# Kernel tuning notes

Hardware: AMD Instinct MI355X
Metric: run time of the kernel (lower is better)

The kernel has to match this reference:

```python
import jax, jax.numpy as jnp
import numpy as np

N = 50000       # nodes
E = 800000      # edges (avg degree 16)
IN_F = 128
OUT_F = 128
NEG_SLOPE = 0.2  # LeakyReLU alpha
EPS = 1e-10


def setup_inputs() -> dict:
    key = jax.random.key(0)
    k1, k2, k3, k4 = jax.random.split(key, 4)
    h = jax.random.normal(k1, (N, IN_F), dtype=jnp.float32)
    edge_index = jax.random.randint(k2, (2, E), 0, N, dtype=jnp.int32)
    # nn.Linear(in, out, bias=False): weight is [out, in], Wh = h @ W.T
    W = jax.random.normal(k3, (OUT_F, IN_F), dtype=jnp.float32) * (1.0 / np.sqrt(IN_F))
    # a: [2*out, 1], xavier_uniform with gain=1.414
    lim = 1.414 * np.sqrt(6.0 / (2 * OUT_F + 1))
    a = jax.random.uniform(k4, (2 * OUT_F, 1), dtype=jnp.float32, minval=-lim, maxval=lim)
    return {"h": h, "edge_index": edge_index, "W": W, "a": a}


def reference(h, edge_index, W, a):
    Wh = h @ W.T                              # [N, out]
    rows = edge_index[0]
    cols = edge_index[1]
    # cat([Wh_i, Wh_j],1) @ a  ==  (Wh @ a1)[rows] + (Wh @ a2)[cols]
    a1 = a[:OUT_F, 0]
    a2 = a[OUT_F:, 0]
    s1 = Wh @ a1                              # [N]
    s2 = Wh @ a2                              # [N]
    e = jax.nn.leaky_relu(s1[rows] + s2[cols], negative_slope=NEG_SLOPE)  # [E]
    e = e - jnp.max(e)
    exp_e = jnp.exp(e)
    sum_exp = jax.ops.segment_sum(exp_e, rows, num_segments=N)            # [N]
    alpha = exp_e / (sum_exp[rows] + EPS)                                 # [E]
    # sparse.mm(adj_att, Wh): h_prime[i] = sum_j alpha_ij * Wh[j]
    h_prime = jax.ops.segment_sum(alpha[:, None] * Wh[cols], rows, num_segments=N)
    return jax.nn.elu(h_prime)
```

## Files before the change

kernel.cpp:

```cpp
#include <hip/hip_runtime.h>

constexpr int FD = 128;
constexpr int NBMAX = 512;
constexpr int CH1 = 2048;
constexpr int CAPB = 3072;

typedef __attribute__((ext_vector_type(8))) short short8;
typedef __attribute__((ext_vector_type(4))) float floatx4;

__device__ __forceinline__ unsigned fenc(float f) {
    unsigned u = __float_as_uint(f);
    return (u & 0x80000000u) ? ~u : (u | 0x80000000u);
}
__device__ __forceinline__ float fdec(unsigned e) {
    return (e & 0x80000000u) ? __uint_as_float(e & 0x7fffffffu)
                             : __uint_as_float(~e);
}

__device__ __forceinline__ unsigned bpack(float x, float y) {
    unsigned ux = __float_as_uint(x); ux += 0x7FFFu + ((ux >> 16) & 1u);
    unsigned uy = __float_as_uint(y); uy += 0x7FFFu + ((uy >> 16) & 1u);
    return (ux >> 16) | (uy & 0xFFFF0000u);
}

__global__ __launch_bounds__(128) void initwt_kernel(const float* __restrict__ W,
                                                     unsigned* __restrict__ Wb,
                                                     int* __restrict__ bhist,
                                                     unsigned* __restrict__ maxslot) {
    int j = blockIdx.x, k = threadIdx.x;
    float w = W[(size_t)j * FD + k];
    float pw = __shfl_xor(w, 1, 64);
    if ((k & 1) == 0) Wb[(size_t)j * 64 + (k >> 1)] = bpack(w, pw);
    if (j == 0) {
        for (int i = k; i < NBMAX; i += 128) bhist[i] = 0;
        if (k < 2) maxslot[k] = 0x007FFFFFu;
    }
}

__global__ __launch_bounds__(256) void gemm_kernel(const float* __restrict__ h,
                                                   const unsigned* __restrict__ Wb,
                                                   const float* __restrict__ a,
                                                   unsigned* __restrict__ Whb,
                                                   float* __restrict__ s1,
                                                   float* __restrict__ s2, int n) {
    int w = threadIdx.x >> 6, lane = threadIdx.x & 63;
    int quad = lane >> 4, c = lane & 15;
    int rbase = blockIdx.x * 64 + w * 16;

    int arow = min(rbase + c, n - 1);
    const float4* hrow = (const float4*)(h + (size_t)arow * FD);
    union { uint4 u; short8 s; } af[4];
#pragma unroll
    for (int kk = 0; kk < 4; ++kk) {
        int k0 = kk * 32 + quad * 8;
        float4 f0 = hrow[k0 >> 2];
        float4 f1 = hrow[(k0 >> 2) + 1];
        af[kk].u.x = bpack(f0.x, f0.y);
        af[kk].u.y = bpack(f0.z, f0.w);
        af[kk].u.z = bpack(f1.x, f1.y);
        af[kk].u.w = bpack(f1.z, f1.w);
    }

    float p1a[4] = {0.f, 0.f, 0.f, 0.f};
    float p2a[4] = {0.f, 0.f, 0.f, 0.f};

#pragma unroll
    for (int t = 0; t < 8; ++t) {
        const uint4* brow = (const uint4*)(Wb + (size_t)(t * 16 + c) * 64 + quad * 4);
        floatx4 acc = {0.f, 0.f, 0.f, 0.f};
#pragma unroll
        for (int kk = 0; kk < 4; ++kk) {
            union { uint4 u; short8 s; } bf;
            bf.u = brow[kk * 4];
            acc = __builtin_amdgcn_mfma_f32_16x16x32_bf16(af[kk].s, bf.s, acc, 0, 0, 0);
        }
        float a1v = a[t * 16 + c];
        float a2v = a[FD + t * 16 + c];
#pragma unroll
        for (int i = 0; i < 4; ++i) {
            float v = acc[i];
            p1a[i] = fmaf(v, a1v, p1a[i]);
            p2a[i] = fmaf(v, a2v, p2a[i]);
            float pv = __shfl_xor(v, 1, 64);
            int r = rbase + quad * 4 + i;
            if ((c & 1) == 0 && r < n)
                Whb[(size_t)r * 64 + t * 8 + (c >> 1)] = bpack(v, pv);
        }
    }

#pragma unroll
    for (int d = 1; d < 16; d <<= 1) {
#pragma unroll
        for (int i = 0; i < 4; ++i) {
            p1a[i] += __shfl_xor(p1a[i], d, 64);
            p2a[i] += __shfl_xor(p2a[i], d, 64);
        }
    }
    if (c == 0) {
#pragma unroll
        for (int i = 0; i < 4; ++i) {
            int r = rbase + quad * 4 + i;
            if (r < n) { s1[r] = p1a[i]; s2[r] = p2a[i]; }
        }
    }
}

__global__ __launch_bounds__(256) void smax_kernel(const float* __restrict__ s1,
                                                   const float* __restrict__ s2,
                                                   unsigned* __restrict__ maxslot, int n) {
    __shared__ float m1s[4], m2s[4];
    int t = threadIdx.x, lane = t & 63, wid = t >> 6;
    float m1 = -3.0e38f, m2 = -3.0e38f;
    for (int i = blockIdx.x * 256 + t; i < n; i += gridDim.x * 256) {
        m1 = fmaxf(m1, s1[i]);
        m2 = fmaxf(m2, s2[i]);
    }
#pragma unroll
    for (int d = 1; d < 64; d <<= 1) {
        m1 = fmaxf(m1, __shfl_xor(m1, d, 64));
        m2 = fmaxf(m2, __shfl_xor(m2, d, 64));
    }
    if (lane == 0) { m1s[wid] = m1; m2s[wid] = m2; }
    __syncthreads();
    if (t == 0) {
        m1 = fmaxf(fmaxf(m1s[0], m1s[1]), fmaxf(m1s[2], m1s[3]));
        m2 = fmaxf(fmaxf(m2s[0], m2s[1]), fmaxf(m2s[2], m2s[3]));
        atomicMax(&maxslot[0], fenc(m1));
        atomicMax(&maxslot[1], fenc(m2));
    }
}

__global__ __launch_bounds__(256) void bhist_kernel(const int* __restrict__ ei,
                                                    int* __restrict__ bhist,
                                                    int e_cnt, int nb) {
    __shared__ int h[NBMAX];
    int t = threadIdx.x;
    for (int i = t; i < NBMAX; i += 256) h[i] = 0;
    __syncthreads();
    int base = blockIdx.x * CH1;
    int m = min(CH1, e_cnt - base);
    for (int idx = t; idx < m; idx += 256) {
        int r = ei[base + idx];
        atomicAdd(&h[r >> 7], 1);
    }
    __syncthreads();
    for (int i = t; i < nb; i += 256)
        if (h[i]) atomicAdd(&bhist[i], h[i]);
}

__global__ __launch_bounds__(512) void bscan_kernel(const int* __restrict__ bhist,
                                                    int* __restrict__ bstart,
                                                    int* __restrict__ bcursor,
                                                    int nb, int e_cnt) {
    __shared__ int sc[512];
    int t = threadIdx.x;
    int v = (t < nb) ? bhist[t] : 0;
    sc[t] = v;
    __syncthreads();
    for (int off = 1; off < 512; off <<= 1) {
        int u = (t >= off) ? sc[t - off] : 0;
        __syncthreads();
        sc[t] += u;
        __syncthreads();
    }
    if (t < nb) {
        int ex = sc[t] - v;
        bstart[t] = ex;
        bcursor[t] = ex;
    }
    if (t == 0) bstart[nb] = e_cnt;
}

__global__ __launch_bounds__(512) void bin_kernel(const int* __restrict__ ei,
                                                  int* __restrict__ bcursor,
                                                  unsigned* __restrict__ ebuf,
                                                  int e_cnt, int nb) {
    __shared__ int cnt[NBMAX];
    __shared__ int ex[NBMAX];
    __shared__ int gbase[NBMAX];
    __shared__ unsigned stage[CH1];
    int t = threadIdx.x;
    cnt[t] = 0;
    __syncthreads();
    int base = blockIdx.x * CH1;
    int m = min(CH1, e_cnt - base);

    unsigned pack[4];
    int rank[4], bkt[4];
    int nk = 0;
#pragma unroll
    for (int k = 0; k < 4; ++k) {
        int idx = t + k * 512;
        if (idx < m) {
            int e = base + idx;
            int r = ei[e];
            int c = ei[e_cnt + e];
            unsigned p = ((unsigned)r << 16) | (unsigned)c;
            int b = r >> 7;
            pack[nk] = p;
            bkt[nk] = b;
            rank[nk] = atomicAdd(&cnt[b], 1);
            ++nk;
        }
    }
    __syncthreads();
    int v = cnt[t];
    ex[t] = v;
    __syncthreads();
    for (int off = 1; off < 512; off <<= 1) {
        int u = (t >= off) ? ex[t - off] : 0;
        __syncthreads();
        ex[t] += u;
        __syncthreads();
    }
    int excl = ex[t] - v;
    if (t < nb && v > 0) gbase[t] = atomicAdd(&bcursor[t], v);
    __syncthreads();
    ex[t] = excl;
    __syncthreads();
    for (int k = 0; k < nk; ++k) stage[ex[bkt[k]] + rank[k]] = pack[k];
    __syncthreads();
    for (int s = t; s < m; s += 512) {
        unsigned p = stage[s];
        int b = p >> 23;
        ebuf[gbase[b] + (s - ex[b])] = p;
    }
}

__global__ __launch_bounds__(1024) void agg_kernel(const unsigned* __restrict__ ebuf,
                                                   const int* __restrict__ bstart,
                                                   const float* __restrict__ s1,
                                                   const float* __restrict__ s2,
                                                   const unsigned* __restrict__ Whb,
                                                   const unsigned* __restrict__ maxslot,
                                                   float* __restrict__ out, int n) {
    __shared__ unsigned stage[CAPB];
    __shared__ float evs[CAPB];
    __shared__ int cnt[128];
    __shared__ int exs[128];
    __shared__ float invs[128];
    __shared__ float s1l[128];
    int b = blockIdx.x;
    int t = threadIdx.x;
    int row0 = b << 7;
    int start = bstart[b];
    int m = min(bstart[b + 1] - start, CAPB);

    if (t < 128) {
        cnt[t] = 0;
        int gr = row0 + t;
        s1l[t] = (gr < n) ? s1[gr] : 0.f;
    }
    __syncthreads();
    for (int i = t; i < m; i += 1024)
        atomicAdd(&cnt[(ebuf[start + i] >> 16) & 127], 1);
    __syncthreads();
    int v = (t < 128) ? cnt[t] : 0;
    if (t < 128) exs[t] = v;
    __syncthreads();
    for (int off = 1; off < 128; off <<= 1) {
        int u = (t < 128 && t >= off) ? exs[t - off] : 0;
        __syncthreads();
        if (t < 128) exs[t] += u;
        __syncthreads();
    }
    if (t < 128) { exs[t] -= v; cnt[t] = 0; }
    __syncthreads();
    for (int i = t; i < m; i += 1024) {
        unsigned p = ebuf[start + i];
        int lr = (p >> 16) & 127;
        int rk = atomicAdd(&cnt[lr], 1);
        stage[exs[lr] + rk] = p;
    }
    __syncthreads();

    float M = fdec(maxslot[0]) + fdec(maxslot[1]);
    M = (M >= 0.f) ? M : 0.2f * M;

    for (int i = t; i < m; i += 1024) {
        unsigned p = stage[i];
        float sv = s1l[(p >> 16) & 127] + s2[p & 0xFFFFu];
        float le = (sv >= 0.f) ? sv : 0.2f * sv;
        evs[i] = expf(le - M);
    }
    __syncthreads();
    if (t < 128) {
        int s0 = exs[t], d = cnt[t];
        float s = 0.f;
        for (int k = 0; k < d; ++k) s += evs[s0 + k];
        invs[t] = 1.0f / (s + 1e-10f);
    }
    __syncthreads();
    for (int i = t; i < m; i += 1024)
        evs[i] *= invs[(stage[i] >> 16) & 127];
    __syncthreads();

    int w = t >> 6, l = t & 63, half = l >> 5, fl = l & 31;
    for (int ni = (w << 3); ni < (w << 3) + 8; ++ni) {
        int node = row0 + ni;
        if (node >= n) break;
        int s0 = exs[ni], deg = cnt[ni];
        float4 acc = make_float4(0.f, 0.f, 0.f, 0.f);
        int j = half;
        for (; j + 2 < deg; j += 4) {
            unsigned c0 = stage[s0 + j] & 0xFFFFu;
            unsigned c1 = stage[s0 + j + 2] & 0xFFFFu;
            float a0 = evs[s0 + j], a1 = evs[s0 + j + 2];
            uint2 b0 = *(const uint2*)(Whb + (size_t)c0 * 64 + 2 * fl);
            uint2 b1 = *(const uint2*)(Whb + (size_t)c1 * 64 + 2 * fl);
            acc.x = fmaf(a0, __uint_as_float(b0.x << 16), acc.x);
            acc.y = fmaf(a0, __uint_as_float(b0.x & 0xFFFF0000u), acc.y);
            acc.z = fmaf(a0, __uint_as_float(b0.y << 16), acc.z);
            acc.w = fmaf(a0, __uint_as_float(b0.y & 0xFFFF0000u), acc.w);
            acc.x = fmaf(a1, __uint_as_float(b1.x << 16), acc.x);
            acc.y = fmaf(a1, __uint_as_float(b1.x & 0xFFFF0000u), acc.y);
            acc.z = fmaf(a1, __uint_as_float(b1.y << 16), acc.z);
            acc.w = fmaf(a1, __uint_as_float(b1.y & 0xFFFF0000u), acc.w);
        }
        if (j < deg) {
            unsigned c0 = stage[s0 + j] & 0xFFFFu;
            float a0 = evs[s0 + j];
            uint2 b0 = *(const uint2*)(Whb + (size_t)c0 * 64 + 2 * fl);
            acc.x = fmaf(a0, __uint_as_float(b0.x << 16), acc.x);
            acc.y = fmaf(a0, __uint_as_float(b0.x & 0xFFFF0000u), acc.y);
            acc.z = fmaf(a0, __uint_as_float(b0.y << 16), acc.z);
            acc.w = fmaf(a0, __uint_as_float(b0.y & 0xFFFF0000u), acc.w);
        }
        acc.x += __shfl_xor(acc.x, 32, 64);
        acc.y += __shfl_xor(acc.y, 32, 64);
        acc.z += __shfl_xor(acc.z, 32, 64);
        acc.w += __shfl_xor(acc.w, 32, 64);
        if (half == 0) {
            float4 r;
            r.x = (acc.x > 0.f) ? acc.x : expm1f(acc.x);
            r.y = (acc.y > 0.f) ? acc.y : expm1f(acc.y);
            r.z = (acc.z > 0.f) ? acc.z : expm1f(acc.z);
            r.w = (acc.w > 0.f) ? acc.w : expm1f(acc.w);
            ((float4*)(out + (size_t)node * FD))[fl] = r;
        }
    }
}

extern "C" void kernel_launch(void* const* d_in, const int* in_sizes, int n_in,
                              void* d_out, int out_size, void* d_ws, size_t ws_size,
                              hipStream_t stream) {
    const float* h = (const float*)d_in[0];
    const int* ei  = (const int*)d_in[1];
    const float* W = (const float*)d_in[2];
    const float* a = (const float*)d_in[3];
    float* out = (float*)d_out;
    int n = in_sizes[0] / FD;
    int e = in_sizes[1] / 2;
    int nb = (n + 127) >> 7;

    char* ws = (char*)d_ws;
    size_t off = 0;
    auto alloc = [&](size_t bytes) -> void* {
        void* p = ws + off;
        off += bytes;
        off = (off + 255) & ~(size_t)255;
        return p;
    };
    unsigned* Whb     = (unsigned*)alloc((size_t)n * 64 * sizeof(unsigned));
    unsigned* Wb      = (unsigned*)alloc((size_t)FD * 64 * sizeof(unsigned));
    float*    s1      = (float*)alloc((size_t)n * sizeof(float));
    float*    s2      = (float*)alloc((size_t)n * sizeof(float));
    int*      bhist   = (int*)alloc((size_t)NBMAX * sizeof(int));
    int*      bstart  = (int*)alloc((size_t)(NBMAX + 1) * sizeof(int));
    int*      bcursor = (int*)alloc((size_t)NBMAX * sizeof(int));
    unsigned* ebuf    = (unsigned*)alloc((size_t)e * sizeof(unsigned));
    unsigned* maxslot = (unsigned*)alloc(2 * sizeof(unsigned));

    int eblocks = (e + CH1 - 1) / CH1;

    initwt_kernel<<<FD, FD, 0, stream>>>(W, Wb, bhist, maxslot);
    bhist_kernel<<<eblocks, 256, 0, stream>>>(ei, bhist, e, nb);
    gemm_kernel<<<(n + 63) / 64, 256, 0, stream>>>(h, Wb, a, Whb, s1, s2, n);
    smax_kernel<<<104, 256, 0, stream>>>(s1, s2, maxslot, n);
    bscan_kernel<<<1, 512, 0, stream>>>(bhist, bstart, bcursor, nb, e);
    bin_kernel<<<eblocks, 512, 0, stream>>>(ei, bcursor, ebuf, e, nb);
    agg_kernel<<<nb, 1024, 0, stream>>>(ebuf, bstart, s1, s2, Whb, maxslot, out, n);
}
```

Measured before the change: 170.5 us.

## Fuse GEMM, max and binning into one kernel with fixed-capacity per-bucket edge buffers

Merges the GEMM, score-max reduction and edge binning into a single launch where blocks split by index into GEMM or binning roles. Drops the histogram and scan kernels by giving each 128-row bucket a fixed CAPB slot in ebuf, so the global offset is just an atomic cursor. The aggregation kernel builds (col, exp) pairs in one pass, sums each row with parallel lanes, and applies the normalization at output. This cuts launches and passes over the edges, but edges beyond CAPB per bucket are silently dropped.

```diff
diff --git a/kernel.cpp b/kernel.cpp
--- a/kernel.cpp
+++ b/kernel.cpp
@@ -25,217 +25,197 @@
 
 __global__ __launch_bounds__(128) void initwt_kernel(const float* __restrict__ W,
                                                      unsigned* __restrict__ Wb,
-                                                     int* __restrict__ bhist,
+                                                     int* __restrict__ bcursor,
                                                      unsigned* __restrict__ maxslot) {
     int j = blockIdx.x, k = threadIdx.x;
     float w = W[(size_t)j * FD + k];
     float pw = __shfl_xor(w, 1, 64);
     if ((k & 1) == 0) Wb[(size_t)j * 64 + (k >> 1)] = bpack(w, pw);
     if (j == 0) {
-        for (int i = k; i < NBMAX; i += 128) bhist[i] = 0;
+        for (int i = k; i < NBMAX; i += 128) bcursor[i] = 0;
         if (k < 2) maxslot[k] = 0x007FFFFFu;
     }
 }
 
-__global__ __launch_bounds__(256) void gemm_kernel(const float* __restrict__ h,
-                                                   const unsigned* __restrict__ Wb,
-                                                   const float* __restrict__ a,
-                                                   unsigned* __restrict__ Whb,
-                                                   float* __restrict__ s1,
-                                                   float* __restrict__ s2, int n) {
-    int w = threadIdx.x >> 6, lane = threadIdx.x & 63;
-    int quad = lane >> 4, c = lane & 15;
-    int rbase = blockIdx.x * 64 + w * 16;
-
-    int arow = min(rbase + c, n - 1);
-    const float4* hrow = (const float4*)(h + (size_t)arow * FD);
-    union { uint4 u; short8 s; } af[4];
-#pragma unroll
-    for (int kk = 0; kk < 4; ++kk) {
-        int k0 = kk * 32 + quad * 8;
-        float4 f0 = hrow[k0 >> 2];
-        float4 f1 = hrow[(k0 >> 2) + 1];
-        af[kk].u.x = bpack(f0.x, f0.y);
-        af[kk].u.y = bpack(f0.z, f0.w);
-        af[kk].u.z = bpack(f1.x, f1.y);
-        af[kk].u.w = bpack(f1.z, f1.w);
-    }
-
-    float p1a[4] = {0.f, 0.f, 0.f, 0.f};
-    float p2a[4] = {0.f, 0.f, 0.f, 0.f};
-
-#pragma unroll
-    for (int t = 0; t < 8; ++t) {
-        const uint4* brow = (const uint4*)(Wb + (size_t)(t * 16 + c) * 64 + quad * 4);
-        floatx4 acc = {0.f, 0.f, 0.f, 0.f};
+union GBShared {
+    struct {
+        int cnt[NBMAX];
+        int ex[NBMAX];
+        int gbase[NBMAX];
+        int wtot[8];
+        unsigned stage[CH1];
+    } bin;
+    struct {
+        float m1[8];
+        float m2[8];
+    } gm;
+};
+
+__global__ __launch_bounds__(512) void gembin_kernel(const float* __restrict__ h,
+                                                     const unsigned* __restrict__ Wb,
+                                                     const float* __restrict__ a,
+                                                     const int* __restrict__ ei,
+                                                     int* __restrict__ bcursor,
+                                                     unsigned* __restrict__ Whb,
+                                                     float* __restrict__ s1,
+                                                     float* __restrict__ s2,
+                                                     unsigned* __restrict__ ebuf,
+                                                     unsigned* __restrict__ maxslot,
+                                                     int n, int e_cnt, int ngemm) {
+    __shared__ GBShared sh;
+    int t = threadIdx.x;
+
+    if ((int)blockIdx.x < ngemm) {
+        int w = t >> 6, lane = t & 63;
+        int quad = lane >> 4, c = lane & 15;
+        int rbase = blockIdx.x * 128 + w * 16;
+
+        int arow = min(rbase + c, n - 1);
+        const float4* hrow = (const float4*)(h + (size_t)arow * FD);
+        union { uint4 u; short8 s; } af[4];
 #pragma unroll
         for (int kk = 0; kk < 4; ++kk) {
-            union { uint4 u; short8 s; } bf;
-            bf.u = brow[kk * 4];
-            acc = __builtin_amdgcn_mfma_f32_16x16x32_bf16(af[kk].s, bf.s, acc, 0, 0, 0);
-        }
-        float a1v = a[t * 16 + c];
-        float a2v = a[FD + t * 16 + c];
-#pragma unroll
-        for (int i = 0; i < 4; ++i) {
-            float v = acc[i];
-            p1a[i] = fmaf(v, a1v, p1a[i]);
-            p2a[i] = fmaf(v, a2v, p2a[i]);
-            float pv = __shfl_xor(v, 1, 64);
-            int r = rbase + quad * 4 + i;
-            if ((c & 1) == 0 && r < n)
-                Whb[(size_t)r * 64 + t * 8 + (c >> 1)] = bpack(v, pv);
-        }
-    }
-
-#pragma unroll
-    for (int d = 1; d < 16; d <<= 1) {
-#pragma unroll
-        for (int i = 0; i < 4; ++i) {
-            p1a[i] += __shfl_xor(p1a[i], d, 64);
-            p2a[i] += __shfl_xor(p2a[i], d, 64);
-        }
-    }
-    if (c == 0) {
+            int k0 = kk * 32 + quad * 8;
+            float4 f0 = hrow[k0 >> 2];
+            float4 f1 = hrow[(k0 >> 2) + 1];
+            af[kk].u.x = bpack(f0.x, f0.y);
+            af[kk].u.y = bpack(f0.z, f0.w);
+            af[kk].u.z = bpack(f1.x, f1.y);
+            af[kk].u.w = bpack(f1.z, f1.w);
+        }
+
+        float p1a[4] = {0.f, 0.f, 0.f, 0.f};
+        float p2a[4] = {0.f, 0.f, 0.f, 0.f};
+
+#pragma unroll
+        for (int tt = 0; tt < 8; ++tt) {
+            const uint4* brow = (const uint4*)(Wb + (size_t)(tt * 16 + c) * 64 + quad * 4);
+            floatx4 acc = {0.f, 0.f, 0.f, 0.f};
+#pragma unroll
+            for (int kk = 0; kk < 4; ++kk) {
+                union { uint4 u; short8 s; } bf;
+                bf.u = brow[kk * 4];
+                acc = __builtin_amdgcn_mfma_f32_16x16x32_bf16(af[kk].s, bf.s, acc, 0, 0, 0);
+            }
+            float a1v = a[tt * 16 + c];
+            float a2v = a[FD + tt * 16 + c];
+#pragma unroll
+            for (int i = 0; i < 4; ++i) {
+                float v = acc[i];
+                p1a[i] = fmaf(v, a1v, p1a[i]);
+                p2a[i] = fmaf(v, a2v, p2a[i]);
+                float pv = __shfl_xor(v, 1, 64);
+                int r = rbase + quad * 4 + i;
+                if ((c & 1) == 0 && r < n)
+                    Whb[(size_t)r * 64 + tt * 8 + (c >> 1)] = bpack(v, pv);
+            }
+        }
+
+#pragma unroll
+        for (int d = 1; d < 16; d <<= 1) {
+#pragma unroll
+            for (int i = 0; i < 4; ++i) {
+                p1a[i] += __shfl_xor(p1a[i], d, 64);
+                p2a[i] += __shfl_xor(p2a[i], d, 64);
+            }
+        }
+        if (c == 0) {
+#pragma unroll
+            for (int i = 0; i < 4; ++i) {
+                int r = rbase + quad * 4 + i;
+                if (r < n) { s1[r] = p1a[i]; s2[r] = p2a[i]; }
+            }
+        }
+
+        float m1 = -3.0e38f, m2 = -3.0e38f;
 #pragma unroll
         for (int i = 0; i < 4; ++i) {
             int r = rbase + quad * 4 + i;
-            if (r < n) { s1[r] = p1a[i]; s2[r] = p2a[i]; }
-        }
-    }
-}
-
-__global__ __launch_bounds__(256) void smax_kernel(const float* __restrict__ s1,
-                                                   const float* __restrict__ s2,
-                                                   unsigned* __restrict__ maxslot, int n) {
-    __shared__ float m1s[4], m2s[4];
-    int t = threadIdx.x, lane = t & 63, wid = t >> 6;
-    float m1 = -3.0e38f, m2 = -3.0e38f;
-    for (int i = blockIdx.x * 256 + t; i < n; i += gridDim.x * 256) {
-        m1 = fmaxf(m1, s1[i]);
-        m2 = fmaxf(m2, s2[i]);
-    }
-#pragma unroll
-    for (int d = 1; d < 64; d <<= 1) {
-        m1 = fmaxf(m1, __shfl_xor(m1, d, 64));
-        m2 = fmaxf(m2, __shfl_xor(m2, d, 64));
-    }
-    if (lane == 0) { m1s[wid] = m1; m2s[wid] = m2; }
-    __syncthreads();
-    if (t == 0) {
-        m1 = fmaxf(fmaxf(m1s[0], m1s[1]), fmaxf(m1s[2], m1s[3]));
-        m2 = fmaxf(fmaxf(m2s[0], m2s[1]), fmaxf(m2s[2], m2s[3]));
-        atomicMax(&maxslot[0], fenc(m1));
-        atomicMax(&maxslot[1], fenc(m2));
-    }
-}
-
-__global__ __launch_bounds__(256) void bhist_kernel(const int* __restrict__ ei,
-                                                    int* __restrict__ bhist,
-                                                    int e_cnt, int nb) {
-    __shared__ int h[NBMAX];
-    int t = threadIdx.x;
-    for (int i = t; i < NBMAX; i += 256) h[i] = 0;
-    __syncthreads();
-    int base = blockIdx.x * CH1;
-    int m = min(CH1, e_cnt - base);
-    for (int idx = t; idx < m; idx += 256) {
-        int r = ei[base + idx];
-        atomicAdd(&h[r >> 7], 1);
-    }
-    __syncthreads();
-    for (int i = t; i < nb; i += 256)
-        if (h[i]) atomicAdd(&bhist[i], h[i]);
-}
-
-__global__ __launch_bounds__(512) void bscan_kernel(const int* __restrict__ bhist,
-                                                    int* __restrict__ bstart,
-                                                    int* __restrict__ bcursor,
-                                                    int nb, int e_cnt) {
-    __shared__ int sc[512];
-    int t = threadIdx.x;
-    int v = (t < nb) ? bhist[t] : 0;
-    sc[t] = v;
-    __syncthreads();
-    for (int off = 1; off < 512; off <<= 1) {
-        int u = (t >= off) ? sc[t - off] : 0;
-        __syncthreads();
-        sc[t] += u;
-        __syncthreads();
-    }
-    if (t < nb) {
-        int ex = sc[t] - v;
-        bstart[t] = ex;
-        bcursor[t] = ex;
-    }
-    if (t == 0) bstart[nb] = e_cnt;
-}
-
-__global__ __launch_bounds__(512) void bin_kernel(const int* __restrict__ ei,
-                                                  int* __restrict__ bcursor,
-                                                  unsigned* __restrict__ ebuf,
-                                                  int e_cnt, int nb) {
-    __shared__ int cnt[NBMAX];
-    __shared__ int ex[NBMAX];
-    __shared__ int gbase[NBMAX];
-    __shared__ unsigned stage[CH1];
-    int t = threadIdx.x;
-    cnt[t] = 0;
-    __syncthreads();
-    int base = blockIdx.x * CH1;
-    int m = min(CH1, e_cnt - base);
-
-    unsigned pack[4];
-    int rank[4], bkt[4];
-    int nk = 0;
-#pragma unroll
-    for (int k = 0; k < 4; ++k) {
-        int idx = t + k * 512;
-        if (idx < m) {
-            int e = base + idx;
-            int r = ei[e];
-            int c = ei[e_cnt + e];
-            unsigned p = ((unsigned)r << 16) | (unsigned)c;
-            int b = r >> 7;
-            pack[nk] = p;
-            bkt[nk] = b;
-            rank[nk] = atomicAdd(&cnt[b], 1);
-            ++nk;
-        }
-    }
-    __syncthreads();
-    int v = cnt[t];
-    ex[t] = v;
-    __syncthreads();
-    for (int off = 1; off < 512; off <<= 1) {
-        int u = (t >= off) ? ex[t - off] : 0;
-        __syncthreads();
-        ex[t] += u;
-        __syncthreads();
-    }
-    int excl = ex[t] - v;
-    if (t < nb && v > 0) gbase[t] = atomicAdd(&bcursor[t], v);
-    __syncthreads();
-    ex[t] = excl;
-    __syncthreads();
-    for (int k = 0; k < nk; ++k) stage[ex[bkt[k]] + rank[k]] = pack[k];
-    __syncthreads();
-    for (int s = t; s < m; s += 512) {
-        unsigned p = stage[s];
-        int b = p >> 23;
-        ebuf[gbase[b] + (s - ex[b])] = p;
+            if (r < n) { m1 = fmaxf(m1, p1a[i]); m2 = fmaxf(m2, p2a[i]); }
+        }
+        m1 = fmaxf(m1, __shfl_xor(m1, 16, 64));
+        m1 = fmaxf(m1, __shfl_xor(m1, 32, 64));
+        m2 = fmaxf(m2, __shfl_xor(m2, 16, 64));
+        m2 = fmaxf(m2, __shfl_xor(m2, 32, 64));
+        if (lane == 0) { sh.gm.m1[w] = m1; sh.gm.m2[w] = m2; }
+        __syncthreads();
+        if (t == 0) {
+            float g1 = -3.0e38f, g2 = -3.0e38f;
+#pragma unroll
+            for (int k = 0; k < 8; ++k) {
+                g1 = fmaxf(g1, sh.gm.m1[k]);
+                g2 = fmaxf(g2, sh.gm.m2[k]);
+            }
+            atomicMax(&maxslot[0], fenc(g1));
+            atomicMax(&maxslot[1], fenc(g2));
+        }
+    } else {
+        int bb = blockIdx.x - ngemm;
+        sh.bin.cnt[t] = 0;
+        __syncthreads();
+        int base = bb * CH1;
+        int m = min(CH1, e_cnt - base);
+
+        unsigned pack[4];
+        int rank[4], bkt[4];
+        int nk = 0;
+#pragma unroll
+        for (int k = 0; k < 4; ++k) {
+            int idx = t + k * 512;
+            if (idx < m) {
+                int ed = base + idx;
+                int r = ei[ed];
+                int cc = ei[e_cnt + ed];
+                unsigned p = ((unsigned)r << 16) | (unsigned)cc;
+                int b = r >> 7;
+                pack[nk] = p;
+                bkt[nk] = b;
+                rank[nk] = atomicAdd(&sh.bin.cnt[b], 1);
+                ++nk;
+            }
+        }
+        __syncthreads();
+
+        int l = t & 63, w = t >> 6;
+        int v = sh.bin.cnt[t];
+        int iv = v;
+#pragma unroll
+        for (int d = 1; d < 64; d <<= 1) {
+            int u = __shfl_up(iv, d, 64);
+            if (l >= d) iv += u;
+        }
+        if (l == 63) sh.bin.wtot[w] = iv;
+        __syncthreads();
+        if (t == 0) {
+            int s = 0;
+#pragma unroll
+            for (int k = 0; k < 8; ++k) { int x = sh.bin.wtot[k]; sh.bin.wtot[k] = s; s += x; }
+        }
+        __syncthreads();
+        int excl = iv - v + sh.bin.wtot[w];
+        sh.bin.ex[t] = excl;
+        if (v > 0) sh.bin.gbase[t] = atomicAdd(&bcursor[t], v);
+        __syncthreads();
+        for (int k = 0; k < nk; ++k)
+            sh.bin.stage[sh.bin.ex[bkt[k]] + rank[k]] = pack[k];
+        __syncthreads();
+        for (int s = t; s < m; s += 512) {
+            unsigned p = sh.bin.stage[s];
+            int b = p >> 23;
+            int pos = sh.bin.gbase[b] + (s - sh.bin.ex[b]);
+            if (pos < CAPB) ebuf[(size_t)b * CAPB + pos] = p;
+        }
     }
 }
 
 __global__ __launch_bounds__(1024) void agg_kernel(const unsigned* __restrict__ ebuf,
-                                                   const int* __restrict__ bstart,
+                                                   const int* __restrict__ bcnt,
                                                    const float* __restrict__ s1,
                                                    const float* __restrict__ s2,
                                                    const unsigned* __restrict__ Whb,
                                                    const unsigned* __restrict__ maxslot,
                                                    float* __restrict__ out, int n) {
-    __shared__ unsigned stage[CAPB];
-    __shared__ float evs[CAPB];
+    __shared__ uint2 pairs[CAPB];
     __shared__ int cnt[128];
     __shared__ int exs[128];
     __shared__ float invs[128];
@@ -243,8 +223,7 @@
     int b = blockIdx.x;
     int t = threadIdx.x;
     int row0 = b << 7;
-    int start = bstart[b];
-    int m = min(bstart[b + 1] - start, CAPB);
+    int m = min(bcnt[b], CAPB);
 
     if (t < 128) {
         cnt[t] = 0;
@@ -252,47 +231,65 @@
         s1l[t] = (gr < n) ? s1[gr] : 0.f;
     }
     __syncthreads();
-    for (int i = t; i < m; i += 1024)
-        atomicAdd(&cnt[(ebuf[start + i] >> 16) & 127], 1);
-    __syncthreads();
-    int v = (t < 128) ? cnt[t] : 0;
-    if (t < 128) exs[t] = v;
-    __syncthreads();
-    for (int off = 1; off < 128; off <<= 1) {
-        int u = (t < 128 && t >= off) ? exs[t - off] : 0;
-        __syncthreads();
-        if (t < 128) exs[t] += u;
-        __syncthreads();
-    }
-    if (t < 128) { exs[t] -= v; cnt[t] = 0; }
-    __syncthreads();
-    for (int i = t; i < m; i += 1024) {
-        unsigned p = ebuf[start + i];
-        int lr = (p >> 16) & 127;
-        int rk = atomicAdd(&cnt[lr], 1);
-        stage[exs[lr] + rk] = p;
+
+    unsigned pk[3];
+    int rk[3], lrr[3];
+    int nk = 0;
+#pragma unroll
+    for (int k = 0; k < 3; ++k) {
+        int idx = t + (k << 10);
+        if (idx < m) {
+            unsigned p = ebuf[(size_t)b * CAPB + idx];
+            int lr = (p >> 16) & 127;
+            pk[nk] = p;
+            lrr[nk] = lr;
+            rk[nk] = atomicAdd(&cnt[lr], 1);
+            ++nk;
+        }
+    }
+    __syncthreads();
+
+    if (t < 64) {
+        int va = cnt[t], vb = cnt[t + 64];
+        int ia = va, ib = vb;
+#pragma unroll
+        for (int d = 1; d < 64; d <<= 1) {
+            int ua = __shfl_up(ia, d, 64);
+            int ub = __shfl_up(ib, d, 64);
+            if (t >= d) { ia += ua; ib += ub; }
+        }
+        int tot = __shfl(ia, 63, 64);
+        exs[t] = ia - va;
+        exs[t + 64] = tot + ib - vb;
     }
     __syncthreads();
 
     float M = fdec(maxslot[0]) + fdec(maxslot[1]);
     M = (M >= 0.f) ? M : 0.2f * M;
 
-    for (int i = t; i < m; i += 1024) {
-        unsigned p = stage[i];
-        float sv = s1l[(p >> 16) & 127] + s2[p & 0xFFFFu];
+    for (int k = 0; k < nk; ++k) {
+        unsigned p = pk[k];
+        int col = p & 0xFFFF;
+        float sv = s1l[lrr[k]] + s2[col];
         float le = (sv >= 0.f) ? sv : 0.2f * sv;
-        evs[i] = expf(le - M);
-    }
-    __syncthreads();
-    if (t < 128) {
-        int s0 = exs[t], d = cnt[t];
-        float s = 0.f;
-        for (int k = 0; k < d; ++k) s += evs[s0 + k];
-        invs[t] = 1.0f / (s + 1e-10f);
-    }
-    __syncthreads();
-    for (int i = t; i < m; i += 1024)
-        evs[i] *= invs[(stage[i] >> 16) & 127];
+        float ev = expf(le - M);
+        pairs[exs[lrr[k]] + rk[k]] = make_uint2((unsigned)col, __float_as_uint(ev));
+    }
+    __syncthreads();
+
+    {
+        int hw = t >> 5, fl = t & 31;
+        for (int r = hw; r < 128; r += 32) {
+            int s0 = exs[r], d = cnt[r];
+            float s = 0.f;
+            for (int k2 = fl; k2 < d; k2 += 32)
+                s += __uint_as_float(pairs[s0 + k2].y);
+#pragma unroll
+            for (int dd = 1; dd < 32; dd <<= 1)
+                s += __shfl_xor(s, dd, 64);
+            if (fl == 0) invs[r] = 1.0f / (s + 1e-10f);
+        }
+    }
     __syncthreads();
 
     int w = t >> 6, l = t & 63, half = l >> 5, fl = l & 31;
@@ -303,11 +300,11 @@
         float4 acc = make_float4(0.f, 0.f, 0.f, 0.f);
         int j = half;
         for (; j + 2 < deg; j += 4) {
-            unsigned c0 = stage[s0 + j] & 0xFFFFu;
-            unsigned c1 = stage[s0 + j + 2] & 0xFFFFu;
-            float a0 = evs[s0 + j], a1 = evs[s0 + j + 2];
-            uint2 b0 = *(const uint2*)(Whb + (size_t)c0 * 64 + 2 * fl);
-            uint2 b1 = *(const uint2*)(Whb + (size_t)c1 * 64 + 2 * fl);
+            uint2 q0 = pairs[s0 + j];
+            uint2 q1 = pairs[s0 + j + 2];
+            float a0 = __uint_as_float(q0.y), a1 = __uint_as_float(q1.y);
+            uint2 b0 = *(const uint2*)(Whb + (size_t)q0.x * 64 + 2 * fl);
+            uint2 b1 = *(const uint2*)(Whb + (size_t)q1.x * 64 + 2 * fl);
             acc.x = fmaf(a0, __uint_as_float(b0.x << 16), acc.x);
             acc.y = fmaf(a0, __uint_as_float(b0.x & 0xFFFF0000u), acc.y);
             acc.z = fmaf(a0, __uint_as_float(b0.y << 16), acc.z);
@@ -318,9 +315,9 @@
             acc.w = fmaf(a1, __uint_as_float(b1.y & 0xFFFF0000u), acc.w);
         }
         if (j < deg) {
-            unsigned c0 = stage[s0 + j] & 0xFFFFu;
-            float a0 = evs[s0 + j];
-            uint2 b0 = *(const uint2*)(Whb + (size_t)c0 * 64 + 2 * fl);
+            uint2 q0 = pairs[s0 + j];
+            float a0 = __uint_as_float(q0.y);
+            uint2 b0 = *(const uint2*)(Whb + (size_t)q0.x * 64 + 2 * fl);
             acc.x = fmaf(a0, __uint_as_float(b0.x << 16), acc.x);
             acc.y = fmaf(a0, __uint_as_float(b0.x & 0xFFFF0000u), acc.y);
             acc.z = fmaf(a0, __uint_as_float(b0.y << 16), acc.z);
@@ -331,11 +328,13 @@
         acc.z += __shfl_xor(acc.z, 32, 64);
         acc.w += __shfl_xor(acc.w, 32, 64);
         if (half == 0) {
+            float inv = invs[ni];
+            float x = acc.x * inv, y = acc.y * inv, z = acc.z * inv, u = acc.w * inv;
             float4 r;
-            r.x = (acc.x > 0.f) ? acc.x : expm1f(acc.x);
-            r.y = (acc.y > 0.f) ? acc.y : expm1f(acc.y);
-            r.z = (acc.z > 0.f) ? acc.z : expm1f(acc.z);
-            r.w = (acc.w > 0.f) ? acc.w : expm1f(acc.w);
+            r.x = (x > 0.f) ? x : expm1f(x);
+            r.y = (y > 0.f) ? y : expm1f(y);
+            r.z = (z > 0.f) ? z : expm1f(z);
+            r.w = (u > 0.f) ? u : expm1f(u);
             ((float4*)(out + (size_t)node * FD))[fl] = r;
         }
     }
@@ -365,19 +364,15 @@
     unsigned* Wb      = (unsigned*)alloc((size_t)FD * 64 * sizeof(unsigned));
     float*    s1      = (float*)alloc((size_t)n * sizeof(float));
     float*    s2      = (float*)alloc((size_t)n * sizeof(float));
-    int*      bhist   = (int*)alloc((size_t)NBMAX * sizeof(int));
-    int*      bstart  = (int*)alloc((size_t)(NBMAX + 1) * sizeof(int));
     int*      bcursor = (int*)alloc((size_t)NBMAX * sizeof(int));
-    unsigned* ebuf    = (unsigned*)alloc((size_t)e * sizeof(unsigned));
+    unsigned* ebuf    = (unsigned*)alloc((size_t)NBMAX * CAPB * sizeof(unsigned));
     unsigned* maxslot = (unsigned*)alloc(2 * sizeof(unsigned));
 
-    int eblocks = (e + CH1 - 1) / CH1;
-
-    initwt_kernel<<<FD, FD, 0, stream>>>(W, Wb, bhist, maxslot);
-    bhist_kernel<<<eblocks, 256, 0, stream>>>(ei, bhist, e, nb);
-    gemm_kernel<<<(n + 63) / 64, 256, 0, stream>>>(h, Wb, a, Whb, s1, s2, n);
-    smax_kernel<<<104, 256, 0, stream>>>(s1, s2, maxslot, n);
-    bscan_kernel<<<1, 512, 0, stream>>>(bhist, bstart, bcursor, nb, e);
-    bin_kernel<<<eblocks, 512, 0, stream>>>(ei, bcursor, ebuf, e, nb);
-    agg_kernel<<<nb, 1024, 0, stream>>>(ebuf, bstart, s1, s2, Whb, maxslot, out, n);
-}
+    int ngemm = (n + 127) / 128;
+    int nbin = (e + CH1 - 1) / CH1;
+
+    initwt_kernel<<<FD, 128, 0, stream>>>(W, Wb, bcursor, maxslot);
+    gembin_kernel<<<ngemm + nbin, 512, 0, stream>>>(h, Wb, a, ei, bcursor, Whb,
+                                                    s1, s2, ebuf, maxslot, n, e, ngemm);
+    agg_kernel<<<nb, 1024, 0, stream>>>(ebuf, bcursor, s1, s2, Whb, maxslot, out, n);
+}
```

Result: faster. 145.0 us (median of 2 runs) (-15.0%).
